# Performance work log

Measured on AMD Instinct MI355X. Metric: run time of the kernel, lower is better.

## Reference

```python
import jax, jax.numpy as jnp
import numpy as np

B, S, D, H = 2, 2048, 1024, 16  # batch, seq_len, model dim, heads


def setup_inputs() -> dict:
    key = jax.random.key(0)
    ks = jax.random.split(key, 5)
    return {
        "x": jax.random.normal(ks[0], (B, S, D), jnp.float32),
        "idx": jax.random.randint(ks[1], (B,), 0, S),
        "weight": jnp.float32(0.5),
        "attn_forcing": 1,  # static python flag
        "w_qkv": jax.random.normal(ks[2], (D, 3 * D), jnp.float32) * 0.02,
        "b_qkv": jnp.zeros((3 * D,), jnp.float32),
        "w_proj": jax.random.normal(ks[3], (D, D), jnp.float32) * 0.02,
        "b_proj": jnp.zeros((D,), jnp.float32),
    }


def reference(x, idx, weight, attn_forcing, w_qkv, b_qkv, w_proj, b_proj):
    Bx, Sx, Dm = x.shape
    dh = Dm // H
    # qkv projection (Conv1D: x @ w + b)
    qkv = x @ w_qkv + b_qkv  # [B,S,3D]
    q, k, v = jnp.split(qkv, 3, axis=-1)
    q = q.reshape(Bx, Sx, H, dh).transpose(0, 2, 1, 3)  # [B,H,S,dh]
    k = k.reshape(Bx, Sx, H, dh).transpose(0, 2, 1, 3)
    v = v.reshape(Bx, Sx, H, dh).transpose(0, 2, 1, 3)
    alen = jnp.arange(Sx)
    mask = (alen[None, :] <= alen[:, None]).astype(x.dtype)  # [S,S] causal
    w = jnp.einsum('bhqd,bhkd->bhqk', q, k) / jnp.asarray(np.sqrt(dh), x.dtype)
    w = w * mask + jnp.asarray(-1e9, x.dtype) * (1 - mask)
    w = jax.nn.softmax(w, axis=-1)
    if attn_forcing:
        # post-softmax forcing reweight: positions >= idx scaled by weight, then renorm
        a = jnp.where(alen[None, :] >= idx[:, None], weight, jnp.asarray(1.0, x.dtype))  # [B,S]
        w = w * a[:, None, None, :]
        w = w / jnp.sum(w, axis=-1, keepdims=True)
    out = jnp.einsum('bhqk,bhkd->bhqd', w, v)  # [B,H,S,dh]
    out = out.transpose(0, 2, 1, 3).reshape(Bx, Sx, Dm)  # merge heads
    return out @ w_proj + b_proj
```

## Files before the change

### kernel.cpp

```cpp
#include <hip/hip_runtime.h>


typedef __attribute__((ext_vector_type(8))) short short8;
typedef __attribute__((ext_vector_type(4))) float f32x4;

#define MFMA_B16(a, b, c) __builtin_amdgcn_mfma_f32_16x16x32_bf16(a, b, c, 0, 0, 0)

#if __has_builtin(__builtin_amdgcn_exp2f)
#define EXP2(x) __builtin_amdgcn_exp2f(x)
#else
#define EXP2(x) exp2f(x)
#endif

static __device__ __forceinline__ unsigned short f2bf(float f) {
    union { float f; unsigned int u; } v;
    v.f = f;
    unsigned int r = (v.u + 0x7fffu + ((v.u >> 16) & 1u)) >> 16;
    return (unsigned short)r;
}

static __device__ __forceinline__ unsigned int pk_bf16(float a, float b) {
#if __has_builtin(__builtin_amdgcn_cvt_pk_bf16_f32)
    typedef __bf16 bf2 __attribute__((ext_vector_type(2)));
    union { bf2 v; unsigned int u; } c;
    c.v = __builtin_amdgcn_cvt_pk_bf16_f32(a, b);
    return c.u;
#else
    return (unsigned int)f2bf(a) | ((unsigned int)f2bf(b) << 16);
#endif
}

static __device__ __forceinline__ void gl_lds16(const void* g, void* l) {
    __builtin_amdgcn_global_load_lds(
        (const __attribute__((address_space(1))) unsigned int*)g,
        (__attribute__((address_space(3))) unsigned int*)l, 16, 0, 0);
}

__global__ __launch_bounds__(256) void prep_kernel(const float4* __restrict__ x,
                                                   uint4* __restrict__ xb,
                                                   const float* __restrict__ wqkv,
                                                   unsigned short* __restrict__ wqkvT,
                                                   const float* __restrict__ wproj,
                                                   unsigned short* __restrict__ wprojT) {
    const int bid = blockIdx.x;
    if (bid < 2048) {
        int i = bid * 256 + threadIdx.x;
        float4 v0 = x[i * 2], v1 = x[i * 2 + 1];
        uint4 o;
        o.x = pk_bf16(v0.x, v0.y);
        o.y = pk_bf16(v0.z, v0.w);
        o.z = pk_bf16(v1.x, v1.y);
        o.w = pk_bf16(v1.z, v1.w);
        xb[i] = o;
        return;
    }
    __shared__ float t[32][33];
    const float* in;
    unsigned short* out;
    int R, C, bx, by;
    if (bid < 2048 + 3072) {
        int g = bid - 2048;
        in = wqkv; out = wqkvT; R = 1024; C = 3072;
        bx = g % 96; by = g / 96;
    } else {
        int g = bid - 5120;
        in = wproj; out = wprojT; R = 1024; C = 1024;
        bx = g & 31; by = g >> 5;
    }
    const int c0 = bx * 32, r0 = by * 32;
    const int xx = threadIdx.x & 31, yy0 = threadIdx.x >> 5;
    #pragma unroll
    for (int yy = yy0; yy < 32; yy += 8)
        t[yy][xx] = in[(size_t)(r0 + yy) * C + (c0 + xx)];
    __syncthreads();
    #pragma unroll
    for (int yy = yy0; yy < 32; yy += 8)
        out[(size_t)(c0 + yy) * R + (r0 + xx)] = f2bf(t[xx][yy]);
}

__global__ __launch_bounds__(256) void gemm_qkv_kernel(const unsigned short* __restrict__ A,
                                                       const unsigned short* __restrict__ Bt,
                                                       const float* __restrict__ bias,
                                                       unsigned short* __restrict__ q,
                                                       unsigned short* __restrict__ k,
                                                       unsigned short* __restrict__ vT) {
    __shared__ unsigned short As[2][8192];
    __shared__ unsigned short Bs[2][8192];
    const int tid = threadIdx.x;
    const int lane = tid & 63, wave = tid >> 6;
    const int l15 = lane & 15, quad = lane >> 4;
    const int wm = wave >> 1, wn = wave & 1;
    const int bid = blockIdx.x;
    const int xcd = bid & 7, jj = bid >> 3;
    const int col = xcd * 3 + jj % 3;
    const int row0 = (jj / 3) * 128, col0 = col * 128;
    const int K = 1024;
    const bool isV = (col >= 16);

    int srow[4], scol[4], sdst[4];
    #pragma unroll
    for (int h = 0; h < 4; ++h) {
        int D = h * 256 + wave * 64 + lane;
        srow[h] = D >> 3;
        scol[h] = ((D & 7) ^ (srow[h] & 7)) * 8;
        sdst[h] = (h * 256 + wave * 64) * 8;
    }

    f32x4 acc[4][4] = {};

    #pragma unroll
    for (int h = 0; h < 4; ++h) {
        gl_lds16(&A[(size_t)(row0 + srow[h]) * K + scol[h]], &As[0][sdst[h]]);
        gl_lds16(&Bt[(size_t)(col0 + srow[h]) * K + scol[h]], &Bs[0][sdst[h]]);
    }
    __syncthreads();

    for (int kt = 0; kt < 16; ++kt) {
        const int cur = kt & 1;
        if (kt + 1 < 16) {
            const int ko = (kt + 1) * 64;
            #pragma unroll
            for (int h = 0; h < 4; ++h) {
                gl_lds16(&A[(size_t)(row0 + srow[h]) * K + ko + scol[h]], &As[cur ^ 1][sdst[h]]);
                gl_lds16(&Bt[(size_t)(col0 + srow[h]) * K + ko + scol[h]], &Bs[cur ^ 1][sdst[h]]);
            }
        }
        #pragma unroll
        for (int kk = 0; kk < 2; ++kk) {
            short8 af[4], bf[4];
            #pragma unroll
            for (int i = 0; i < 4; ++i) {
                int r = wm * 64 + i * 16 + l15;
                af[i] = *(const short8*)&As[cur][r * 64 + (((kk * 4 + quad) ^ (r & 7)) * 8)];
            }
            #pragma unroll
            for (int j = 0; j < 4; ++j) {
                int r = wn * 64 + j * 16 + l15;
                bf[j] = *(const short8*)&Bs[cur][r * 64 + (((kk * 4 + quad) ^ (r & 7)) * 8)];
            }
            if (isV) {
                #pragma unroll
                for (int i = 0; i < 4; ++i)
                    #pragma unroll
                    for (int j = 0; j < 4; ++j)
                        acc[i][j] = MFMA_B16(af[i], bf[j], acc[i][j]);
            } else {
                #pragma unroll
                for (int i = 0; i < 4; ++i)
                    #pragma unroll
                    for (int j = 0; j < 4; ++j)
                        acc[i][j] = MFMA_B16(bf[j], af[i], acc[i][j]);
            }
        }
        __syncthreads();
    }

    const int b = row0 >> 11;
    const int s0 = row0 & 2047;
    const float* bb = bias + col0 + wn * 64;

    if (!isV) {
        const int which = col >> 3;
        unsigned short* dst = which ? k : q;
        const float scale = which ? 1.0f : 0.1803368867f;
        const int hh = ((col & 7) << 1) + wn;
        #pragma unroll
        for (int i = 0; i < 4; ++i) {
            const int s = s0 + wm * 64 + i * 16 + l15;
            unsigned short* drow = dst + ((size_t)((b * 16 + hh) * 2048 + s)) * 64;
            #pragma unroll
            for (int j = 0; j < 4; ++j) {
                float4 b4 = ((const float4*)bb)[j * 4 + quad];
                uint2 pv;
                pv.x = pk_bf16((acc[i][j][0] + b4.x) * scale, (acc[i][j][1] + b4.y) * scale);
                pv.y = pk_bf16((acc[i][j][2] + b4.z) * scale, (acc[i][j][3] + b4.w) * scale);
                *(uint2*)&drow[j * 16 + quad * 4] = pv;
            }
        }
    } else {
        const int hh = ((col - 16) << 1) + wn;
        #pragma unroll
        for (int j = 0; j < 4; ++j) {
            const int d = j * 16 + l15;
            const float bv = bb[d];
            unsigned short* drow = vT + ((size_t)((b * 16 + hh) * 64 + d)) * 2048 + s0;
            #pragma unroll
            for (int i = 0; i < 4; ++i) {
                uint2 pv;
                pv.x = pk_bf16(acc[i][j][0] + bv, acc[i][j][1] + bv);
                pv.y = pk_bf16(acc[i][j][2] + bv, acc[i][j][3] + bv);
                *(uint2*)&drow[wm * 64 + i * 16 + quad * 4] = pv;
            }
        }
    }
}

__global__ __launch_bounds__(256) void gemm_proj_kernel(const unsigned short* __restrict__ A,
                                                        const unsigned short* __restrict__ Bt,
                                                        const float* __restrict__ bias,
                                                        float* __restrict__ out) {
    __shared__ unsigned short As[2][8192];
    __shared__ unsigned short Bs[2][4096];
    const int tid = threadIdx.x;
    const int lane = tid & 63, wave = tid >> 6;
    const int l15 = lane & 15, quad = lane >> 4;
    const int wm = wave >> 1, wn = wave & 1;
    const int bid = blockIdx.x;
    const int xcd = bid & 7, jj = bid >> 3;
    const int colb = xcd * 2 + (jj & 1);
    const int row0 = (jj >> 1) * 128, col0 = colb * 64;
    const int K = 1024;

    int srow[4], scol[4], sdst[4];
    #pragma unroll
    for (int h = 0; h < 4; ++h) {
        int D = h * 256 + wave * 64 + lane;
        srow[h] = D >> 3;
        scol[h] = ((D & 7) ^ (srow[h] & 7)) * 8;
        sdst[h] = (h * 256 + wave * 64) * 8;
    }

    f32x4 acc[4][2] = {};

    #pragma unroll
    for (int h = 0; h < 4; ++h)
        gl_lds16(&A[(size_t)(row0 + srow[h]) * K + scol[h]], &As[0][sdst[h]]);
    #pragma unroll
    for (int h = 0; h < 2; ++h)
        gl_lds16(&Bt[(size_t)(col0 + srow[h]) * K + scol[h]], &Bs[0][sdst[h]]);
    __syncthreads();

    for (int kt = 0; kt < 16; ++kt) {
        const int cur = kt & 1;
        if (kt + 1 < 16) {
            const int ko = (kt + 1) * 64;
            #pragma unroll
            for (int h = 0; h < 4; ++h)
                gl_lds16(&A[(size_t)(row0 + srow[h]) * K + ko + scol[h]], &As[cur ^ 1][sdst[h]]);
            #pragma unroll
            for (int h = 0; h < 2; ++h)
                gl_lds16(&Bt[(size_t)(col0 + srow[h]) * K + ko + scol[h]], &Bs[cur ^ 1][sdst[h]]);
        }
        #pragma unroll
        for (int kk = 0; kk < 2; ++kk) {
            short8 af[4], bf[2];
            #pragma unroll
            for (int i = 0; i < 4; ++i) {
                int r = wm * 64 + i * 16 + l15;
                af[i] = *(const short8*)&As[cur][r * 64 + (((kk * 4 + quad) ^ (r & 7)) * 8)];
            }
            #pragma unroll
            for (int j = 0; j < 2; ++j) {
                int r = wn * 32 + j * 16 + l15;
                bf[j] = *(const short8*)&Bs[cur][r * 64 + (((kk * 4 + quad) ^ (r & 7)) * 8)];
            }
            #pragma unroll
            for (int i = 0; i < 4; ++i)
                #pragma unroll
                for (int j = 0; j < 2; ++j)
                    acc[i][j] = MFMA_B16(bf[j], af[i], acc[i][j]);
        }
        __syncthreads();
    }

    const float* bb = bias + col0 + wn * 32;
    #pragma unroll
    for (int i = 0; i < 4; ++i) {
        const int row = row0 + wm * 64 + i * 16 + l15;
        #pragma unroll
        for (int j = 0; j < 2; ++j) {
            float4 b4 = ((const float4*)bb)[j * 4 + quad];
            float4 ov;
            ov.x = acc[i][j][0] + b4.x;
            ov.y = acc[i][j][1] + b4.y;
            ov.z = acc[i][j][2] + b4.z;
            ov.w = acc[i][j][3] + b4.w;
            *(float4*)&out[(size_t)row * 1024 + col0 + wn * 32 + j * 16 + quad * 4] = ov;
        }
    }
}

__global__ __launch_bounds__(512) void attn_kernel(const unsigned short* __restrict__ Q,
                                                   const unsigned short* __restrict__ Kg,
                                                   const unsigned short* __restrict__ Vt,
                                                   const int* __restrict__ idx,
                                                   const float* __restrict__ weight,
                                                   const int* __restrict__ forcing,
                                                   unsigned short* __restrict__ O) {
    __shared__ unsigned short smem[24576];

    const int tid = threadIdx.x;
    const int lane = tid & 63, wave = tid >> 6;
    const int l15 = lane & 15, quad = lane >> 4;
    const int bid = blockIdx.x;
    const int qh = bid >> 8;
    const int rem = bid & 255;
    const int xcd = rem & 7;
    const int head = (rem >> 3) & 3;
    const int g2 = rem >> 5;
    const int p = qh ? (7 - g2) : (8 + g2);
    const int bh = xcd * 4 + head;
    const int tA = 2 * p + 1, tB = 2 * p;
    const int b = bh >> 4, hh = bh & 15;
    const unsigned short* Qb = Q + (size_t)bh * 2048 * 64;
    const unsigned short* Kh = Kg + (size_t)bh * 2048 * 64;
    const unsigned short* Vh = Vt + (size_t)bh * 2048 * 64;

    const int idxb = idx[b];
    const float lw = (forcing[0] != 0) ? __log2f(weight[0]) : 0.0f;

    const int wq = (wave < 4) ? tA : tB;
    const int wg = wave & 3;
    const int q0 = wq * 64 + wg * 16;
    const int qrow = q0 + l15;
    const int nkb = tA + 1;
    const int nkbw = wq + 1;

    const int rS = tid >> 3;
    const int cS8 = ((tid & 7) ^ (rS & 7)) * 8;

    short8 aq0 = *(const short8*)&Qb[(q0 + l15) * 64 + quad * 8];
    short8 aq1 = *(const short8*)&Qb[(q0 + l15) * 64 + 32 + quad * 8];

    const short8 ones8 = {0x3F80, 0x3F80, 0x3F80, 0x3F80, 0x3F80, 0x3F80, 0x3F80, 0x3F80};

    f32x4 o[4] = {};
    f32x4 lsum = {};

    gl_lds16(Kh + (size_t)rS * 64 + cS8,   &smem[tid * 8]);
    gl_lds16(Vh + (size_t)rS * 2048 + cS8, &smem[8192 + tid * 8]);
    __syncthreads();

    unsigned short* const pwb = &smem[16384 + wave * 1024];
    const int pwr = l15 * 64;
    const int pa7 = l15 & 7;

    for (int kb = 0; kb < nkb; ++kb) {
        const int cur = kb & 1;
        const int kbase = kb * 64;
        if (kb + 1 < nkb) {
            const int nb = kbase + 64;
            gl_lds16(Kh + (size_t)(nb + rS) * 64 + cS8,      &smem[(cur ^ 1) * 4096 + tid * 8]);
            gl_lds16(Vh + (size_t)rS * 2048 + nb + cS8,      &smem[8192 + (cur ^ 1) * 4096 + tid * 8]);
        }

        if (kb < nkbw) {
            const unsigned short* KsP = &smem[cur * 4096];
            const unsigned short* VsP = &smem[8192 + cur * 4096];

            const bool fullF = (kbase >= idxb);
            const bool bndF = (!fullF) && (kbase + 63 >= idxb);
            const float zu = fullF ? lw : 0.0f;

            f32x4 sT[4];
            #pragma unroll
            for (int kt = 0; kt < 4; ++kt) {
                const int row = kt * 16 + l15;
                short8 k0 = *(const short8*)&KsP[row * 64 + ((quad ^ (row & 7)) * 8)];
                short8 k1 = *(const short8*)&KsP[row * 64 + (((4 + quad) ^ (row & 7)) * 8)];
                f32x4 z;
                if (!bndF) {
                    z[0] = zu; z[1] = zu; z[2] = zu; z[3] = zu;
                } else {
                    #pragma unroll
                    for (int r = 0; r < 4; ++r)
                        z[r] = (kbase + kt * 16 + quad * 4 + r >= idxb) ? lw : 0.0f;
                }
                z = MFMA_B16(k0, aq0, z);
                z = MFMA_B16(k1, aq1, z);
                sT[kt] = z;
            }

            if (kb == wq) {
                #pragma unroll
                for (int kt = 0; kt < 4; ++kt)
                    #pragma unroll
                    for (int r = 0; r < 4; ++r)
                        if (kbase + kt * 16 + quad * 4 + r > qrow) sT[kt][r] = -3.0e38f;
            }

            #pragma unroll
            for (int kt = 0; kt < 4; ++kt)
                #pragma unroll
                for (int r = 0; r < 4; ++r)
                    sT[kt][r] = EXP2(sT[kt][r]);

            #pragma unroll
            for (int kt = 0; kt < 4; ++kt) {
                unsigned int* pw = (unsigned int*)&pwb[pwr +
                    (((kt * 2 + (quad >> 1)) ^ pa7) * 8) + (quad & 1) * 4];
                pw[0] = pk_bf16(sT[kt][0], sT[kt][1]);
                pw[1] = pk_bf16(sT[kt][2], sT[kt][3]);
            }

            short8 bp0 = *(const short8*)&pwb[pwr + ((quad ^ pa7) * 8)];
            short8 bp1 = *(const short8*)&pwb[pwr + (((4 + quad) ^ pa7) * 8)];

            lsum = MFMA_B16(ones8, bp0, lsum);
            lsum = MFMA_B16(ones8, bp1, lsum);

            #pragma unroll
            for (int dt = 0; dt < 4; ++dt) {
                const int row = dt * 16 + l15;
                short8 vf0 = *(const short8*)&VsP[row * 64 + ((quad ^ (row & 7)) * 8)];
                short8 vf1 = *(const short8*)&VsP[row * 64 + (((4 + quad) ^ (row & 7)) * 8)];
                f32x4 oo = o[dt];
                oo = MFMA_B16(vf0, bp0, oo);
                oo = MFMA_B16(vf1, bp1, oo);
                o[dt] = oo;
            }
        }

        __syncthreads();
    }

    const float inv = 1.0f / lsum[0];
    unsigned short* sc = &smem[wave * 1152];
    #pragma unroll
    for (int dt = 0; dt < 4; ++dt)
        #pragma unroll
        for (int r = 0; r < 4; ++r)
            sc[l15 * 72 + dt * 16 + quad * 4 + r] = f2bf(o[dt][r] * inv);
    const size_t rowoff = ((size_t)(b * 2048 + q0 + l15)) * 1024 + hh * 64;
    #pragma unroll
    for (int h = 0; h < 2; ++h) {
        short8 v8 = *(const short8*)&sc[l15 * 72 + quad * 16 + h * 8];
        *(short8*)&O[rowoff + quad * 16 + h * 8] = v8;
    }
}

extern "C" void kernel_launch(void* const* d_in, const int* in_sizes, int n_in,
                              void* d_out, int out_size, void* d_ws, size_t ws_size,
                              hipStream_t stream) {
    const float* x        = (const float*)d_in[0];
    const int*   idx      = (const int*)d_in[1];
    const float* weight   = (const float*)d_in[2];
    const int*   forcing  = (const int*)d_in[3];
    const float* w_qkv    = (const float*)d_in[4];
    const float* b_qkv    = (const float*)d_in[5];
    const float* w_proj   = (const float*)d_in[6];
    const float* b_proj   = (const float*)d_in[7];
    float* out = (float*)d_out;

    char* ws = (char*)d_ws;
    unsigned short* xb      = (unsigned short*)(ws);
    unsigned short* wqkvT   = (unsigned short*)(ws + 8388608);
    unsigned short* wprojT  = (unsigned short*)(ws + 14680064);
    unsigned short* qbuf    = (unsigned short*)(ws + 16777216);
    unsigned short* kbuf    = (unsigned short*)(ws + 25165824);
    unsigned short* vTbuf   = (unsigned short*)(ws + 33554432);
    unsigned short* attn_out = xb;

    prep_kernel<<<6144, 256, 0, stream>>>((const float4*)x, (uint4*)xb,
                                          w_qkv, wqkvT, w_proj, wprojT);
    gemm_qkv_kernel<<<768, 256, 0, stream>>>(xb, wqkvT, b_qkv, qbuf, kbuf, vTbuf);
    attn_kernel<<<512, 512, 0, stream>>>(qbuf, kbuf, vTbuf, idx, weight, forcing, attn_out);
    gemm_proj_kernel<<<512, 256, 0, stream>>>(attn_out, wprojT, b_proj, out);
}
```

Baseline: 185.1 us.

## Enlarge QKV GEMM tiles to 256x256 with interleaved staged loads and priority MFMA

The QKV projection GEMM moves from 128x128 tiles with 4 waves to 256x256 tiles with 8 waves. It uses 128KB of LDS and launches 192 blocks instead of 768. Global-to-LDS loads are split into half-tile stages and interleaved between four MFMA sub-blocks, with explicit vmcnt waits and barriers, and s_setprio raises priority around the MFMA groups. The aim is more data reuse per block and better overlap of memory with compute. In exchange, 192 blocks is below one wave of work per CU on a 256-CU part, and the larger tile raises register pressure.

```diff
diff --git a/kernel.cpp b/kernel.cpp
--- a/kernel.cpp
+++ b/kernel.cpp
@@ -78,95 +78,138 @@
         out[(size_t)(c0 + yy) * R + (r0 + xx)] = f2bf(t[xx][yy]);
 }
 
-__global__ __launch_bounds__(256) void gemm_qkv_kernel(const unsigned short* __restrict__ A,
+__global__ __launch_bounds__(512) void gemm_qkv_kernel(const unsigned short* __restrict__ A,
                                                        const unsigned short* __restrict__ Bt,
                                                        const float* __restrict__ bias,
                                                        unsigned short* __restrict__ q,
                                                        unsigned short* __restrict__ k,
                                                        unsigned short* __restrict__ vT) {
-    __shared__ unsigned short As[2][8192];
-    __shared__ unsigned short Bs[2][8192];
+    __shared__ unsigned short As[2][16384];
+    __shared__ unsigned short Bs[2][16384];
     const int tid = threadIdx.x;
-    const int lane = tid & 63, wave = tid >> 6;
+    const int lane = tid & 63;
+    const int wave = tid >> 6;
     const int l15 = lane & 15, quad = lane >> 4;
-    const int wm = wave >> 1, wn = wave & 1;
+    const int wm = wave >> 2, wn = wave & 3;
     const int bid = blockIdx.x;
-    const int xcd = bid & 7, jj = bid >> 3;
-    const int col = xcd * 3 + jj % 3;
-    const int row0 = (jj / 3) * 128, col0 = col * 128;
+    const int colblk = bid >> 4, rowblk = bid & 15;
+    const int row0 = rowblk * 256, col0 = colblk * 256;
     const int K = 1024;
-    const bool isV = (col >= 16);
-
-    int srow[4], scol[4], sdst[4];
-    #pragma unroll
-    for (int h = 0; h < 4; ++h) {
-        int D = h * 256 + wave * 64 + lane;
-        srow[h] = D >> 3;
-        scol[h] = ((D & 7) ^ (srow[h] & 7)) * 8;
-        sdst[h] = (h * 256 + wave * 64) * 8;
-    }
-
-    f32x4 acc[4][4] = {};
-
-    #pragma unroll
-    for (int h = 0; h < 4; ++h) {
-        gl_lds16(&A[(size_t)(row0 + srow[h]) * K + scol[h]], &As[0][sdst[h]]);
-        gl_lds16(&Bt[(size_t)(col0 + srow[h]) * K + scol[h]], &Bs[0][sdst[h]]);
-    }
-    __syncthreads();
+    const int sel = col0 >> 10;
+    const bool isV = (sel == 2);
+
+    const int sr = tid >> 3;
+    const int c8 = tid & 7;
+
+    auto stageA = [&](int buf, int h, int kt) {
+        #pragma unroll
+        for (int g = 0; g < 2; ++g) {
+            const int r = g * 64 + sr;
+            const int cs = c8 ^ (r & 7);
+            gl_lds16(&A[(size_t)(row0 + h * 128 + r) * K + kt * 64 + cs * 8],
+                     &As[buf][h * 8192 + g * 4096 + tid * 8]);
+        }
+    };
+    auto stageB = [&](int buf, int h, int kt) {
+        #pragma unroll
+        for (int g = 0; g < 2; ++g) {
+            const int r = g * 64 + sr;
+            const int cs = c8 ^ (r & 7);
+            gl_lds16(&Bt[(size_t)(col0 + h * 128 + r) * K + kt * 64 + cs * 8],
+                     &Bs[buf][h * 8192 + g * 4096 + tid * 8]);
+        }
+    };
+
+    f32x4 acc[8][4] = {};
+
+    stageB(0, 0, 0); stageB(0, 1, 0);
+    stageA(0, 0, 0); stageA(0, 1, 0);
+    stageB(1, 0, 1); stageB(1, 1, 1);
+
+#define LOAD_AF(IBASE)                                                                   \
+    _Pragma("unroll") for (int i = 0; i < 4; ++i) {                                      \
+        const int r = wm * 128 + ((IBASE) + i) * 16 + l15;                               \
+        _Pragma("unroll") for (int kk = 0; kk < 2; ++kk)                                 \
+            afr[i][kk] = *(const short8*)&Ac[r * 64 + (((kk * 4 + quad) ^ (r & 7)) * 8)];\
+    }
+#define LOAD_BF(JBASE)                                                                   \
+    _Pragma("unroll") for (int j = 0; j < 2; ++j) {                                      \
+        const int r = wn * 64 + ((JBASE) + j) * 16 + l15;                                 \
+        _Pragma("unroll") for (int kk = 0; kk < 2; ++kk)                                 \
+            bfr[(JBASE) + j][kk] =                                                       \
+                *(const short8*)&Bc[r * 64 + (((kk * 4 + quad) ^ (r & 7)) * 8)];         \
+    }
+#define MFMA_SET(ILO, JLO)                                                               \
+    __builtin_amdgcn_s_setprio(1);                                                       \
+    if (isV) {                                                                           \
+        _Pragma("unroll") for (int i = 0; i < 4; ++i)                                    \
+        _Pragma("unroll") for (int j = 0; j < 2; ++j) {                                  \
+            acc[(ILO) + i][(JLO) + j] =                                                  \
+                MFMA_B16(afr[i][0], bfr[(JLO) + j][0], acc[(ILO) + i][(JLO) + j]);       \
+            acc[(ILO) + i][(JLO) + j] =                                                  \
+                MFMA_B16(afr[i][1], bfr[(JLO) + j][1], acc[(ILO) + i][(JLO) + j]);       \
+        }                                                                                \
+    } else {                                                                             \
+        _Pragma("unroll") for (int i = 0; i < 4; ++i)                                    \
+        _Pragma("unroll") for (int j = 0; j < 2; ++j) {                                  \
+            acc[(ILO) + i][(JLO) + j] =                                                  \
+                MFMA_B16(bfr[(JLO) + j][0], afr[i][0], acc[(ILO) + i][(JLO) + j]);       \
+            acc[(ILO) + i][(JLO) + j] =                                                  \
+                MFMA_B16(bfr[(JLO) + j][1], afr[i][1], acc[(ILO) + i][(JLO) + j]);       \
+        }                                                                                \
+    }                                                                                    \
+    __builtin_amdgcn_s_setprio(0);
 
     for (int kt = 0; kt < 16; ++kt) {
         const int cur = kt & 1;
-        if (kt + 1 < 16) {
-            const int ko = (kt + 1) * 64;
-            #pragma unroll
-            for (int h = 0; h < 4; ++h) {
-                gl_lds16(&A[(size_t)(row0 + srow[h]) * K + ko + scol[h]], &As[cur ^ 1][sdst[h]]);
-                gl_lds16(&Bt[(size_t)(col0 + srow[h]) * K + ko + scol[h]], &Bs[cur ^ 1][sdst[h]]);
-            }
-        }
-        #pragma unroll
-        for (int kk = 0; kk < 2; ++kk) {
-            short8 af[4], bf[4];
-            #pragma unroll
-            for (int i = 0; i < 4; ++i) {
-                int r = wm * 64 + i * 16 + l15;
-                af[i] = *(const short8*)&As[cur][r * 64 + (((kk * 4 + quad) ^ (r & 7)) * 8)];
-            }
-            #pragma unroll
-            for (int j = 0; j < 4; ++j) {
-                int r = wn * 64 + j * 16 + l15;
-                bf[j] = *(const short8*)&Bs[cur][r * 64 + (((kk * 4 + quad) ^ (r & 7)) * 8)];
-            }
-            if (isV) {
-                #pragma unroll
-                for (int i = 0; i < 4; ++i)
-                    #pragma unroll
-                    for (int j = 0; j < 4; ++j)
-                        acc[i][j] = MFMA_B16(af[i], bf[j], acc[i][j]);
-            } else {
-                #pragma unroll
-                for (int i = 0; i < 4; ++i)
-                    #pragma unroll
-                    for (int j = 0; j < 4; ++j)
-                        acc[i][j] = MFMA_B16(bf[j], af[i], acc[i][j]);
-            }
-        }
-        __syncthreads();
-    }
+        if (kt == 15) {
+            asm volatile("s_waitcnt vmcnt(0)" ::: "memory");
+        } else {
+            asm volatile("s_waitcnt vmcnt(4)" ::: "memory");
+        }
+        __builtin_amdgcn_s_barrier();
+        __builtin_amdgcn_sched_barrier(0);
+
+        const unsigned short* Ac = As[cur];
+        const unsigned short* Bc = Bs[cur];
+
+        short8 afr[4][2], bfr[4][2];
+
+        LOAD_AF(0)
+        LOAD_BF(0)
+        if (kt + 1 < 16) stageA(cur ^ 1, 0, kt + 1);
+        MFMA_SET(0, 0)
+        __builtin_amdgcn_s_barrier();
+
+        LOAD_BF(2)
+        if (kt + 1 < 16) stageA(cur ^ 1, 1, kt + 1);
+        MFMA_SET(0, 2)
+        __builtin_amdgcn_s_barrier();
+
+        LOAD_AF(4)
+        if (kt + 2 < 16) stageB(cur, 0, kt + 2);
+        MFMA_SET(4, 2)
+        __builtin_amdgcn_s_barrier();
+
+        if (kt + 2 < 16) stageB(cur, 1, kt + 2);
+        MFMA_SET(4, 0)
+    }
+
+#undef LOAD_AF
+#undef LOAD_BF
+#undef MFMA_SET
 
     const int b = row0 >> 11;
     const int s0 = row0 & 2047;
+    const int hh = ((col0 & 1023) >> 6) + wn;
     const float* bb = bias + col0 + wn * 64;
 
     if (!isV) {
-        const int which = col >> 3;
-        unsigned short* dst = which ? k : q;
-        const float scale = which ? 1.0f : 0.1803368867f;
-        const int hh = ((col & 7) << 1) + wn;
-        #pragma unroll
-        for (int i = 0; i < 4; ++i) {
-            const int s = s0 + wm * 64 + i * 16 + l15;
+        unsigned short* dst = (sel == 1) ? k : q;
+        const float scale = (sel == 1) ? 1.0f : 0.1803368867f;
+        #pragma unroll
+        for (int i = 0; i < 8; ++i) {
+            const int s = s0 + wm * 128 + i * 16 + l15;
             unsigned short* drow = dst + ((size_t)((b * 16 + hh) * 2048 + s)) * 64;
             #pragma unroll
             for (int j = 0; j < 4; ++j) {
@@ -178,18 +221,17 @@
             }
         }
     } else {
-        const int hh = ((col - 16) << 1) + wn;
         #pragma unroll
         for (int j = 0; j < 4; ++j) {
             const int d = j * 16 + l15;
             const float bv = bb[d];
             unsigned short* drow = vT + ((size_t)((b * 16 + hh) * 64 + d)) * 2048 + s0;
             #pragma unroll
-            for (int i = 0; i < 4; ++i) {
+            for (int i = 0; i < 8; ++i) {
                 uint2 pv;
                 pv.x = pk_bf16(acc[i][j][0] + bv, acc[i][j][1] + bv);
                 pv.y = pk_bf16(acc[i][j][2] + bv, acc[i][j][3] + bv);
-                *(uint2*)&drow[wm * 64 + i * 16 + quad * 4] = pv;
+                *(uint2*)&drow[wm * 128 + i * 16 + quad * 4] = pv;
             }
         }
     }
@@ -453,7 +495,7 @@
 
     prep_kernel<<<6144, 256, 0, stream>>>((const float4*)x, (uint4*)xb,
                                           w_qkv, wqkvT, w_proj, wprojT);
-    gemm_qkv_kernel<<<768, 256, 0, stream>>>(xb, wqkvT, b_qkv, qbuf, kbuf, vTbuf);
+    gemm_qkv_kernel<<<192, 512, 0, stream>>>(xb, wqkvT, b_qkv, qbuf, kbuf, vTbuf);
     attn_kernel<<<512, 512, 0, stream>>>(qbuf, kbuf, vTbuf, idx, weight, forcing, attn_out);
     gemm_proj_kernel<<<512, 256, 0, stream>>>(attn_out, wprojT, b_proj, out);
 }
```

Result: slower. 188.9 us (+2.1%).
